# Optimization experiments

Hardware: AMD Instinct MI355X
Metric: run time of the kernel (lower is better)

## Reference

```python
import jax, jax.numpy as jnp
import numpy as np

B, S, D_IN, D, H, HD, HALF, L = 64, 500, 64, 128, 8, 16, 5, 2
WIN = 2 * HALF + 1  # 11 attended positions per query
EPS = 1e-12  # HF layer_norm_eps default


def _ln(x, g, b):
    m = x.mean(-1, keepdims=True)
    v = ((x - m) ** 2).mean(-1, keepdims=True)
    return (x - m) / jnp.sqrt(v + EPS) * g + b


def setup_inputs() -> dict:
    key = jax.random.key(0)
    ks = jax.random.split(key, 24)
    n = lambda i, shape: jax.random.normal(ks[i], shape, jnp.float32) * 0.02
    return {
        "x": jax.random.normal(ks[0], (B, S, D_IN), jnp.float32),
        "W_in": n(1, (D_IN, D)), "b_in": jnp.zeros((D,), jnp.float32),
        "pos_emb": n(2, (512, D)), "tt_emb": n(3, (D,)),
        "ln_emb_g": jnp.ones((D,), jnp.float32), "ln_emb_b": jnp.zeros((D,), jnp.float32),
        "Wq": n(4, (L, D, D)), "bq": jnp.zeros((L, D), jnp.float32),
        "Wk": n(5, (L, D, D)), "bk": jnp.zeros((L, D), jnp.float32),
        "Wv": n(6, (L, D, D)), "bv": jnp.zeros((L, D), jnp.float32),
        "Wo": n(7, (L, D, D)), "bo": jnp.zeros((L, D), jnp.float32),
        "ln1_g": jnp.ones((L, D), jnp.float32), "ln1_b": jnp.zeros((L, D), jnp.float32),
        "Wi": n(8, (L, D, 512)), "bi": jnp.zeros((L, 512), jnp.float32),
        "Wo2": n(9, (L, 512, D)), "bo2": jnp.zeros((L, D), jnp.float32),
        "ln2_g": jnp.ones((L, D), jnp.float32), "ln2_b": jnp.zeros((L, D), jnp.float32),
        "W_cls": n(10, (D, 2)), "b_cls": jnp.zeros((2,), jnp.float32),
    }


def reference(x, W_in, b_in, pos_emb, tt_emb, ln_emb_g, ln_emb_b,
              Wq, bq, Wk, bk, Wv, bv, Wo, bo, ln1_g, ln1_b,
              Wi, bi, Wo2, bo2, ln2_g, ln2_b, W_cls, b_cls):
    # input projection + RoBERTa-style embeddings (position ids start at padding_idx+1=2)
    h = x @ W_in + b_in
    pos_ids = 2 + jnp.arange(S)
    h = _ln(h + pos_emb[pos_ids] + tt_emb, ln_emb_g, ln_emb_b)

    # sliding-window gather indices: each query attends [i-HALF, i+HALF]
    idx = jnp.arange(S)[:, None] + jnp.arange(-HALF, HALF + 1)[None, :]
    valid = (idx >= 0) & (idx < S)
    idxc = jnp.clip(idx, 0, S - 1)
    scale = 1.0 / jnp.sqrt(jnp.float32(HD))

    for l in range(L):
        qh = (h @ Wq[l] + bq[l]).reshape(B, S, H, HD).transpose(0, 2, 1, 3)
        kh = (h @ Wk[l] + bk[l]).reshape(B, S, H, HD).transpose(0, 2, 1, 3)
        vh = (h @ Wv[l] + bv[l]).reshape(B, S, H, HD).transpose(0, 2, 1, 3)
        kk = kh[:, :, idxc]
        scores = jnp.einsum('bhsd,bhswd->bhsw', qh * scale, kk)
        scores = jnp.where(valid, scores, -jnp.inf)
        probs = jax.nn.softmax(scores, axis=-1)
        vv = vh[:, :, idxc]
        ctx = jnp.einsum('bhsw,bhswd->bhsd', probs, vv)
        ctx = ctx.transpose(0, 2, 1, 3).reshape(B, S, D)
        h = _ln(ctx @ Wo[l] + bo[l] + h, ln1_g[l], ln1_b[l])
        ff = jax.nn.gelu(h @ Wi[l] + bi[l], approximate=False) @ Wo2[l] + bo2[l]
        h = _ln(ff + h, ln2_g[l], ln2_b[l])

    pooled = h.mean(axis=1)  # mean over sequence
    return pooled @ W_cls + b_cls
```

## Files before the change

kernel.cpp:

```cpp
#include <hip/hip_runtime.h>
#include <hip/hip_bf16.h>
#include <math.h>

#define BB 64
#define SS 500
#define DIN 64
#define DD 128
#define HH 8
#define HDIM 16
#define HALF_ 5
#define WINW 11
#define LL 2
#define FF 512
#define MM (BB*SS)
#define LN_EPS 1e-12f

typedef __attribute__((ext_vector_type(8))) short short8;
typedef __attribute__((ext_vector_type(4))) float f32x4;

__global__ __launch_bounds__(256) void k_prep(
    const float* __restrict__ Wq, const float* __restrict__ Wk,
    const float* __restrict__ Wv, const float* __restrict__ Wo,
    const float* __restrict__ Wi, const float* __restrict__ Wo2,
    const float* __restrict__ Win, __hip_bfloat16* __restrict__ wT)
{
    const int m = blockIdx.y;
    const float* src; int Kd, Nd, kshift, doff;
    if (m == 12) {
        src = Win; Kd = 64; Nd = 128; kshift = 6; doff = 393216;
    } else {
        const int l = m / 6, t = m % 6;
        int toff;
        switch (t) {
          case 0:  src = Wq  + l*16384; Kd=128; Nd=128; kshift=7; toff=0;      break;
          case 1:  src = Wk  + l*16384; Kd=128; Nd=128; kshift=7; toff=16384;  break;
          case 2:  src = Wv  + l*16384; Kd=128; Nd=128; kshift=7; toff=32768;  break;
          case 3:  src = Wo  + l*16384; Kd=128; Nd=128; kshift=7; toff=49152;  break;
          case 4:  src = Wi  + l*65536; Kd=128; Nd=512; kshift=7; toff=65536;  break;
          default: src = Wo2 + l*65536; Kd=512; Nd=128; kshift=9; toff=131072; break;
        }
        doff = l*196608 + toff;
    }
    __hip_bfloat16* dst = wT + doff;
    const int NK = Kd * Nd;
    int e = (blockIdx.x * 256 + threadIdx.x) * 4;
    if (e >= NK) return;
    #pragma unroll
    for (int j = 0; j < 4; ++j, ++e) {
        int n = e >> kshift, kx = e & (Kd - 1);
        dst[(size_t)n * Kd + kx] = __float2bfloat16(src[(size_t)kx * Nd + n]);
    }
}

__global__ __launch_bounds__(256) void k_xcvt(
    const float* __restrict__ x, __hip_bfloat16* __restrict__ xbf)
{
    int i = (blockIdx.x * 256 + threadIdx.x) * 4;
    if (i >= MM * DIN) return;
    float4 v = *(const float4*)(x + i);
    ushort4 o;
    __hip_bfloat16 t0 = __float2bfloat16(v.x); o.x = *(unsigned short*)&t0;
    __hip_bfloat16 t1 = __float2bfloat16(v.y); o.y = *(unsigned short*)&t1;
    __hip_bfloat16 t2 = __float2bfloat16(v.z); o.z = *(unsigned short*)&t2;
    __hip_bfloat16 t3 = __float2bfloat16(v.w); o.w = *(unsigned short*)&t3;
    *(ushort4*)(xbf + i) = o;
}

#define GEMM_MAIN(Abf, lda, Kdim, WTbf, ldw, n0w)                             \
    __shared__ __align__(16) __hip_bfloat16 As[64][72];                       \
    __shared__ __align__(16) __hip_bfloat16 Ws[128][72];                      \
    const int tid = threadIdx.x;                                              \
    const int wid = tid >> 6;                                                 \
    const int l15 = tid & 15;                                                 \
    const int l4  = (tid & 63) >> 4;                                          \
    const int m0  = blockIdx.x * 64;                                          \
    f32x4 acc[8];                                                             \
    _Pragma("unroll")                                                         \
    for (int n = 0; n < 8; ++n) acc[n] = (f32x4){0.f, 0.f, 0.f, 0.f};         \
    for (int k0 = 0; k0 < (Kdim); k0 += 64) {                                 \
        _Pragma("unroll")                                                     \
        for (int it = 0; it < 2; ++it) {                                      \
            int lin = it * 2048 + tid * 8;                                    \
            int r = lin >> 6, c = lin & 63;                                   \
            *(uint4*)&As[r][c] =                                              \
                *(const uint4*)((Abf) + (size_t)(m0 + r) * (lda) + k0 + c);   \
        }                                                                     \
        _Pragma("unroll")                                                     \
        for (int it = 0; it < 4; ++it) {                                      \
            int lin = it * 2048 + tid * 8;                                    \
            int r = lin >> 6, c = lin & 63;                                   \
            *(uint4*)&Ws[r][c] =                                              \
                *(const uint4*)((WTbf) + (size_t)((n0w) + r) * (ldw) + k0 + c); \
        }                                                                     \
        __syncthreads();                                                      \
        _Pragma("unroll")                                                     \
        for (int kc = 0; kc < 64; kc += 32) {                                 \
            short8 a0 = *(const short8*)&As[wid * 16 + l15][kc + l4 * 8];     \
            _Pragma("unroll")                                                 \
            for (int n = 0; n < 8; ++n) {                                     \
                short8 bf = *(const short8*)&Ws[n * 16 + l15][kc + l4 * 8];   \
                acc[n] = __builtin_amdgcn_mfma_f32_16x16x32_bf16(a0, bf, acc[n], 0, 0, 0); \
            }                                                                 \
        }                                                                     \
        __syncthreads();                                                      \
    }

__global__ __launch_bounds__(256, 4) void k_embed(
    const __hip_bfloat16* __restrict__ xbf, const __hip_bfloat16* __restrict__ wInT,
    const float* __restrict__ bin, const float* __restrict__ pos,
    const float* __restrict__ tt, const float* __restrict__ g,
    const float* __restrict__ be, float* __restrict__ h,
    __hip_bfloat16* __restrict__ hbf)
{
    GEMM_MAIN(xbf, DIN, DIN, wInT, DIN, 0)
    #pragma unroll
    for (int qq = 0; qq < 4; ++qq) {
        const int row = m0 + wid * 16 + l4 * 4 + qq;
        const int s = row % SS;
        float vals[8]; float s1 = 0.f, s2 = 0.f;
        #pragma unroll
        for (int n = 0; n < 8; ++n) {
            const int col = n * 16 + l15;
            float val = acc[n][qq] + bin[col] + tt[col] + pos[(size_t)(2 + s) * DD + col];
            vals[n] = val; s1 += val; s2 += val * val;
        }
        #pragma unroll
        for (int o = 1; o < 16; o <<= 1) {
            s1 += __shfl_xor(s1, o, 16);
            s2 += __shfl_xor(s2, o, 16);
        }
        const float mean = s1 * (1.0f / DD);
        const float var  = s2 * (1.0f / DD) - mean * mean;
        const float rstd = rsqrtf(var + LN_EPS);
        #pragma unroll
        for (int n = 0; n < 8; ++n) {
            const int col = n * 16 + l15;
            const float o = (vals[n] - mean) * rstd * g[col] + be[col];
            h[(size_t)row * DD + col]   = o;
            hbf[(size_t)row * DD + col] = __float2bfloat16(o);
        }
    }
}

__global__ __launch_bounds__(512, 4) void k_fused(
    const __hip_bfloat16* __restrict__ hin,
    const __hip_bfloat16* __restrict__ wTq, const __hip_bfloat16* __restrict__ wTk,
    const __hip_bfloat16* __restrict__ wTv, const __hip_bfloat16* __restrict__ wTo,
    const float* __restrict__ bq, const float* __restrict__ bk,
    const float* __restrict__ bv, const float* __restrict__ bo,
    const float* __restrict__ hres,
    const float* __restrict__ g1, const float* __restrict__ bt1,
    float* __restrict__ hout, __hip_bfloat16* __restrict__ hbfout)
{
    __shared__ __align__(16) char smem[48896];
    __hip_bfloat16* kS   = (__hip_bfloat16*)smem;
    __hip_bfloat16* vS   = (__hip_bfloat16*)(smem + 13056);
    __hip_bfloat16* hS   = (__hip_bfloat16*)(smem + 26112);
    __hip_bfloat16* qS   = (__hip_bfloat16*)(smem + 39168);
    float*          rsum = (float*)(smem + 47872);
    __hip_bfloat16* ctxS = hS;

    const int tid = threadIdx.x;
    const int wid = tid >> 6;
    const int l15 = tid & 15, l4 = (tid & 63) >> 4;
    const int b = blockIdx.y;
    const int s0 = blockIdx.x * 32;

    #pragma unroll
    for (int it = 0; it < 2; ++it) {
        int lin = it * 512 + tid;
        if (lin < 768) {
            int r = lin >> 4, c8 = (lin & 15) * 8;
            int s = s0 - 5 + r;
            uint4 val = {0, 0, 0, 0};
            if (s >= 0 && s < SS)
                val = *(const uint4*)(hin + ((size_t)(b * SS + s)) * DD + c8);
            *(uint4*)&hS[r * 136 + c8] = val;
        }
    }
    __syncthreads();

    #pragma unroll
    for (int i = 0; i < 9; ++i) {
        const int t = wid + i * 8;
        const int out = t / 24;
        const int rem = t - out * 24;
        const int rt = rem >> 3, n = rem & 7;
        const __hip_bfloat16* WT = (out == 0) ? wTq : ((out == 1) ? wTk : wTv);
        const float* bias = (out == 0) ? bq : ((out == 1) ? bk : bv);
        f32x4 a = (f32x4){0.f, 0.f, 0.f, 0.f};
        #pragma unroll
        for (int kc = 0; kc < 4; ++kc) {
            short8 af  = *(const short8*)&hS[(rt * 16 + l15) * 136 + kc * 32 + l4 * 8];
            short8 bfg = *(const short8*)(WT + (size_t)(n * 16 + l15) * DD + kc * 32 + l4 * 8);
            a = __builtin_amdgcn_mfma_f32_16x16x32_bf16(af, bfg, a, 0, 0, 0);
        }
        const int col = n * 16 + l15;
        const float bcol = bias[col];
        #pragma unroll
        for (int qq = 0; qq < 4; ++qq) {
            const int row = rt * 16 + l4 * 4 + qq;
            const float val = a[qq] + bcol;
            if (out == 0) {
                if (row >= 5 && row < 37)
                    qS[(row - 5) * 136 + col] = __float2bfloat16(val * 0.25f);
            } else if (out == 1) {
                kS[row * 136 + col] = __float2bfloat16(val);
            } else {
                vS[row * 136 + col] = __float2bfloat16(val);
            }
        }
    }
    __syncthreads();

    {
        const int g = tid >> 4, wl = tid & 15;
        const int sq = s0 + g;
        const int sk = sq + wl - HALF_;
        const bool valid = (wl < WINW) && (sq < SS) && (sk >= 0) && (sk < SS);
        #pragma unroll
        for (int hh = 0; hh < 8; ++hh) {
            const int off = hh * 16;
            const uint4* qp = (const uint4*)&qS[g * 136 + off];
            const uint4* kp = (const uint4*)&kS[(g + wl) * 136 + off];
            uint4 qv0 = qp[0], qv1 = qp[1];
            uint4 kv0 = kp[0], kv1 = kp[1];
            float sc = 0.f;
            #define DOTD(qu, ku)                                              \
                sc += __uint_as_float((qu) << 16) * __uint_as_float((ku) << 16) \
                    + __uint_as_float((qu) & 0xffff0000u) * __uint_as_float((ku) & 0xffff0000u);
            DOTD(qv0.x, kv0.x) DOTD(qv0.y, kv0.y) DOTD(qv0.z, kv0.z) DOTD(qv0.w, kv0.w)
            DOTD(qv1.x, kv1.x) DOTD(qv1.y, kv1.y) DOTD(qv1.z, kv1.z) DOTD(qv1.w, kv1.w)
            #undef DOTD
            sc = valid ? sc : -INFINITY;
            float mx = sc;
            #pragma unroll
            for (int o = 1; o < 16; o <<= 1) mx = fmaxf(mx, __shfl_xor(mx, o, 16));
            float p = valid ? __expf(sc - mx) : 0.f;
            float den = p;
            #pragma unroll
            for (int o = 1; o < 16; o <<= 1) den += __shfl_xor(den, o, 16);
            const float inv = (den > 0.f) ? 1.f / den : 0.f;
            float cd = 0.f;
            #pragma unroll
            for (int w2 = 0; w2 < WINW; ++w2)
                cd += __shfl(p, w2, 16) * __bfloat162float(vS[(g + w2) * 136 + off + wl]);
            ctxS[g * 136 + off + wl] = __float2bfloat16(cd * inv);
        }
    }
    __syncthreads();

    const int rt2 = wid & 1, nh = wid >> 1;
    f32x4 ac[2];
    #pragma unroll
    for (int n4 = 0; n4 < 2; ++n4) {
        ac[n4] = (f32x4){0.f, 0.f, 0.f, 0.f};
        const int n = nh * 2 + n4;
        #pragma unroll
        for (int kc = 0; kc < 4; ++kc) {
            short8 af  = *(const short8*)&ctxS[(rt2 * 16 + l15) * 136 + kc * 32 + l4 * 8];
            short8 bfg = *(const short8*)(wTo + (size_t)(n * 16 + l15) * DD + kc * 32 + l4 * 8);
            ac[n4] = __builtin_amdgcn_mfma_f32_16x16x32_bf16(af, bfg, ac[n4], 0, 0, 0);
        }
    }
    float vals[4][2];
    #pragma unroll
    for (int qq = 0; qq < 4; ++qq) {
        const int r16 = l4 * 4 + qq;
        const int qrow = rt2 * 16 + r16;
        const int sq = s0 + qrow;
        const bool vr = (sq < SS);
        float s1 = 0.f, s2 = 0.f;
        #pragma unroll
        for (int n4 = 0; n4 < 2; ++n4) {
            const int col = (nh * 2 + n4) * 16 + l15;
            const float resv = vr ? hres[((size_t)(b * SS + sq)) * DD + col] : 0.f;
            const float val = ac[n4][qq] + bo[col] + resv;
            vals[qq][n4] = val; s1 += val; s2 += val * val;
        }
        #pragma unroll
        for (int o = 1; o < 16; o <<= 1) {
            s1 += __shfl_xor(s1, o, 16);
            s2 += __shfl_xor(s2, o, 16);
        }
        if (l15 == 0) {
            rsum[((rt2 * 4 + nh) * 16 + r16) * 2]     = s1;
            rsum[((rt2 * 4 + nh) * 16 + r16) * 2 + 1] = s2;
        }
    }
    __syncthreads();
    #pragma unroll
    for (int qq = 0; qq < 4; ++qq) {
        const int r16 = l4 * 4 + qq;
        const int qrow = rt2 * 16 + r16;
        const int sq = s0 + qrow;
        if (sq >= SS) continue;
        float S1 = 0.f, S2 = 0.f;
        #pragma unroll
        for (int j = 0; j < 4; ++j) {
            S1 += rsum[((rt2 * 4 + j) * 16 + r16) * 2];
            S2 += rsum[((rt2 * 4 + j) * 16 + r16) * 2 + 1];
        }
        const float mean = S1 * (1.0f / DD);
        const float var  = S2 * (1.0f / DD) - mean * mean;
        const float rstd = rsqrtf(fmaxf(var, 0.f) + LN_EPS);
        #pragma unroll
        for (int n4 = 0; n4 < 2; ++n4) {
            const int col = (nh * 2 + n4) * 16 + l15;
            const float o = (vals[qq][n4] - mean) * rstd * g1[col] + bt1[col];
            hout[((size_t)(b * SS + sq)) * DD + col]   = o;
            hbfout[((size_t)(b * SS + sq)) * DD + col] = __float2bfloat16(o);
        }
    }
}

__global__ __launch_bounds__(256, 4) void k_gemm_gelu(
    const __hip_bfloat16* __restrict__ hbf,
    const __hip_bfloat16* __restrict__ wTi,
    const float* __restrict__ bias, __hip_bfloat16* __restrict__ hid)
{
    const int n0g = blockIdx.y * 128;
    GEMM_MAIN(hbf, DD, DD, wTi, DD, n0g)
    #pragma unroll
    for (int qq = 0; qq < 4; ++qq) {
        const int row = m0 + wid * 16 + l4 * 4 + qq;
        #pragma unroll
        for (int n = 0; n < 8; ++n) {
            const int col = n0g + n * 16 + l15;
            float val = acc[n][qq] + bias[col];
            val = 0.5f * val * (1.f + erff(val * 0.70710678118f));
            hid[(size_t)row * FF + col] = __float2bfloat16(val);
        }
    }
}

__global__ __launch_bounds__(256, 4) void k_gemm_lnres(
    const __hip_bfloat16* __restrict__ Abf, int lda, int Kdim,
    const __hip_bfloat16* __restrict__ WT,
    const float* __restrict__ bias, const float* __restrict__ res,
    const float* __restrict__ g, const float* __restrict__ bt,
    float* __restrict__ outF, __hip_bfloat16* __restrict__ outB)
{
    GEMM_MAIN(Abf, lda, Kdim, WT, Kdim, 0)
    #pragma unroll
    for (int qq = 0; qq < 4; ++qq) {
        const int row = m0 + wid * 16 + l4 * 4 + qq;
        float vals[8]; float s1 = 0.f, s2 = 0.f;
        #pragma unroll
        for (int n = 0; n < 8; ++n) {
            const int col = n * 16 + l15;
            float val = acc[n][qq] + bias[col] + res[(size_t)row * DD + col];
            vals[n] = val; s1 += val; s2 += val * val;
        }
        #pragma unroll
        for (int o = 1; o < 16; o <<= 1) {
            s1 += __shfl_xor(s1, o, 16);
            s2 += __shfl_xor(s2, o, 16);
        }
        const float mean = s1 * (1.0f / DD);
        const float var  = s2 * (1.0f / DD) - mean * mean;
        const float rstd = rsqrtf(var + LN_EPS);
        #pragma unroll
        for (int n = 0; n < 8; ++n) {
            const int col = n * 16 + l15;
            const float o = (vals[n] - mean) * rstd * g[col] + bt[col];
            outF[(size_t)row * DD + col] = o;
            outB[(size_t)row * DD + col] = __float2bfloat16(o);
        }
    }
}

__global__ __launch_bounds__(512) void k_final(
    const float* __restrict__ h, const float* __restrict__ Wc,
    const float* __restrict__ bc, float* __restrict__ out)
{
    const int b = blockIdx.x;
    const int tid = threadIdx.x;
    const int d = tid & 127, sg = tid >> 7;
    __shared__ float red[4][128];
    __shared__ float r2[8][2];

    float p = 0.f;
    for (int s = sg; s < SS; s += 4)
        p += h[((size_t)(b * SS + s)) * DD + d];
    red[sg][d] = p;
    __syncthreads();

    float l0 = 0.f, l1 = 0.f;
    if (sg == 0) {
        const float tot = (red[0][d] + red[1][d] + red[2][d] + red[3][d]) * (1.0f / SS);
        l0 = tot * Wc[d * 2 + 0];
        l1 = tot * Wc[d * 2 + 1];
    }
    #pragma unroll
    for (int off = 1; off < 64; off <<= 1) {
        l0 += __shfl_xor(l0, off);
        l1 += __shfl_xor(l1, off);
    }
    const int w = tid >> 6;
    if ((tid & 63) == 0) { r2[w][0] = l0; r2[w][1] = l1; }
    __syncthreads();
    if (tid == 0) {
        out[b * 2 + 0] = r2[0][0] + r2[1][0] + bc[0];
        out[b * 2 + 1] = r2[0][1] + r2[1][1] + bc[1];
    }
}

extern "C" void kernel_launch(void* const* d_in, const int* in_sizes, int n_in,
                              void* d_out, int out_size, void* d_ws, size_t ws_size,
                              hipStream_t stream)
{
    const float* x      = (const float*)d_in[0];
    const float* W_in   = (const float*)d_in[1];
    const float* b_in   = (const float*)d_in[2];
    const float* pos    = (const float*)d_in[3];
    const float* tt     = (const float*)d_in[4];
    const float* lng    = (const float*)d_in[5];
    const float* lnb    = (const float*)d_in[6];
    const float* Wq     = (const float*)d_in[7];
    const float* bq     = (const float*)d_in[8];
    const float* Wk     = (const float*)d_in[9];
    const float* bk     = (const float*)d_in[10];
    const float* Wv     = (const float*)d_in[11];
    const float* bv     = (const float*)d_in[12];
    const float* Wo     = (const float*)d_in[13];
    const float* bo     = (const float*)d_in[14];
    const float* ln1g   = (const float*)d_in[15];
    const float* ln1b   = (const float*)d_in[16];
    const float* Wi     = (const float*)d_in[17];
    const float* bi     = (const float*)d_in[18];
    const float* Wo2    = (const float*)d_in[19];
    const float* bo2    = (const float*)d_in[20];
    const float* ln2g   = (const float*)d_in[21];
    const float* ln2b   = (const float*)d_in[22];
    const float* Wc     = (const float*)d_in[23];
    const float* bc     = (const float*)d_in[24];

    float*          ws   = (float*)d_ws;
    float*          hA   = ws;
    __hip_bfloat16* hbA  = (__hip_bfloat16*)(ws + 4096000);
    __hip_bfloat16* xbf  = (__hip_bfloat16*)(ws + 6144000);
    __hip_bfloat16* wT   = (__hip_bfloat16*)(ws + 7168000);
    __hip_bfloat16* hid  = (__hip_bfloat16*)(ws + 7368704);
    float*          hB   = ws + 15560704;
    __hip_bfloat16* hbB  = (__hip_bfloat16*)(ws + 19656704);

    k_prep<<<dim3(64, 13), 256, 0, stream>>>(Wq, Wk, Wv, Wo, Wi, Wo2, W_in, wT);
    k_xcvt<<<2000, 256, 0, stream>>>(x, xbf);
    k_embed<<<MM / 64, 256, 0, stream>>>(xbf, wT + 393216, b_in, pos, tt, lng, lnb,
                                         hA, hbA);

    float* hI = hA; __hip_bfloat16* hbI = hbA;
    float* hO = hB; __hip_bfloat16* hbO = hbB;
    for (int l = 0; l < LL; ++l) {
        const __hip_bfloat16* wTq  = wT + l * 196608;
        const __hip_bfloat16* wTk  = wTq + 16384;
        const __hip_bfloat16* wTv  = wTq + 32768;
        const __hip_bfloat16* wTo  = wTq + 49152;
        const __hip_bfloat16* wTi  = wTq + 65536;
        const __hip_bfloat16* wTo2 = wTq + 131072;

        k_fused<<<dim3(16, BB), 512, 0, stream>>>(
            hbI, wTq, wTk, wTv, wTo,
            bq + l * DD, bk + l * DD, bv + l * DD, bo + l * DD,
            hI, ln1g + l * DD, ln1b + l * DD, hO, hbO);

        k_gemm_gelu<<<dim3(MM / 64, 4), 256, 0, stream>>>(
            hbO, wTi, bi + l * FF, hid);

        k_gemm_lnres<<<dim3(MM / 64, 1), 256, 0, stream>>>(
            hid, FF, FF, wTo2, bo2 + l * DD, hO, ln2g + l * DD, ln2b + l * DD,
            hO, hbO);

        float* tf = hI; hI = hO; hO = tf;
        __hip_bfloat16* tb = hbI; hbI = hbO; hbO = tb;
    }

    k_final<<<BB, 512, 0, stream>>>(hI, Wc, bc, (float*)d_out);
}
```

Baseline: 362.3 us.

## Fuse FFN up-projection, GELU and down-projection into one kernel via LDS

Replaces the separate GELU GEMM and LN-residual GEMM kernels with one fused FFN kernel. The 512-wide hidden activation is computed in two 256-column halves, kept in shared memory and consumed immediately by the down-projection. This removes the global round trip of the hidden tensor and one launch per layer. It also drops the global-memory A-tile staging of GEMM_MAIN, and weight B fragments are read straight from global memory. A second change in the attention kernel replaces the shuffle-based broadcast of softmax probabilities with a small shared-memory buffer and uses scalar dword loads for the q·k dot product.

Result: no change. 369.1 us (+1.9%).

```diff
diff --git a/kernel.cpp b/kernel.cpp
--- a/kernel.cpp
+++ b/kernel.cpp
@@ -152,12 +152,13 @@
     const float* __restrict__ g1, const float* __restrict__ bt1,
     float* __restrict__ hout, __hip_bfloat16* __restrict__ hbfout)
 {
-    __shared__ __align__(16) char smem[48896];
+    __shared__ __align__(16) char smem[51072];
     __hip_bfloat16* kS   = (__hip_bfloat16*)smem;
     __hip_bfloat16* vS   = (__hip_bfloat16*)(smem + 13056);
     __hip_bfloat16* hS   = (__hip_bfloat16*)(smem + 26112);
     __hip_bfloat16* qS   = (__hip_bfloat16*)(smem + 39168);
-    float*          rsum = (float*)(smem + 47872);
+    float*          pS   = (float*)(smem + 47872);
+    float*          rsum = (float*)(smem + 50048);
     __hip_bfloat16* ctxS = hS;
 
     const int tid = threadIdx.x;
@@ -221,17 +222,15 @@
         #pragma unroll
         for (int hh = 0; hh < 8; ++hh) {
             const int off = hh * 16;
-            const uint4* qp = (const uint4*)&qS[g * 136 + off];
-            const uint4* kp = (const uint4*)&kS[(g + wl) * 136 + off];
-            uint4 qv0 = qp[0], qv1 = qp[1];
-            uint4 kv0 = kp[0], kv1 = kp[1];
             float sc = 0.f;
-            #define DOTD(qu, ku)                                              \
-                sc += __uint_as_float((qu) << 16) * __uint_as_float((ku) << 16) \
-                    + __uint_as_float((qu) & 0xffff0000u) * __uint_as_float((ku) & 0xffff0000u);
-            DOTD(qv0.x, kv0.x) DOTD(qv0.y, kv0.y) DOTD(qv0.z, kv0.z) DOTD(qv0.w, kv0.w)
-            DOTD(qv1.x, kv1.x) DOTD(qv1.y, kv1.y) DOTD(qv1.z, kv1.z) DOTD(qv1.w, kv1.w)
-            #undef DOTD
+            const unsigned* qp = (const unsigned*)&qS[g * 136 + off];
+            const unsigned* kp = (const unsigned*)&kS[(g + wl) * 136 + off];
+            #pragma unroll
+            for (int d2 = 0; d2 < 8; ++d2) {
+                unsigned qu = qp[d2], ku = kp[d2];
+                sc += __uint_as_float(qu << 16) * __uint_as_float(ku << 16)
+                    + __uint_as_float(qu & 0xffff0000u) * __uint_as_float(ku & 0xffff0000u);
+            }
             sc = valid ? sc : -INFINITY;
             float mx = sc;
             #pragma unroll
@@ -241,10 +240,11 @@
             #pragma unroll
             for (int o = 1; o < 16; o <<= 1) den += __shfl_xor(den, o, 16);
             const float inv = (den > 0.f) ? 1.f / den : 0.f;
+            pS[g * 17 + wl] = p;
             float cd = 0.f;
             #pragma unroll
             for (int w2 = 0; w2 < WINW; ++w2)
-                cd += __shfl(p, w2, 16) * __bfloat162float(vS[(g + w2) * 136 + off + wl]);
+                cd += pS[g * 17 + w2] * __bfloat162float(vS[(g + w2) * 136 + off + wl]);
             ctxS[g * 136 + off + wl] = __float2bfloat16(cd * inv);
         }
     }
@@ -314,34 +314,68 @@
     }
 }
 
-__global__ __launch_bounds__(256, 4) void k_gemm_gelu(
-    const __hip_bfloat16* __restrict__ hbf,
-    const __hip_bfloat16* __restrict__ wTi,
-    const float* __restrict__ bias, __hip_bfloat16* __restrict__ hid)
-{
-    const int n0g = blockIdx.y * 128;
-    GEMM_MAIN(hbf, DD, DD, wTi, DD, n0g)
-    #pragma unroll
-    for (int qq = 0; qq < 4; ++qq) {
-        const int row = m0 + wid * 16 + l4 * 4 + qq;
+__global__ __launch_bounds__(256, 4) void k_ffn(
+    const __hip_bfloat16* __restrict__ h1bf,
+    const __hip_bfloat16* __restrict__ wTi, const __hip_bfloat16* __restrict__ wTo2,
+    const float* __restrict__ bi, const float* __restrict__ bo2,
+    const float* __restrict__ res,
+    const float* __restrict__ g2, const float* __restrict__ bt2,
+    float* __restrict__ outF, __hip_bfloat16* __restrict__ outB)
+{
+    __shared__ __align__(16) __hip_bfloat16 h1S[64][136];
+    __shared__ __align__(16) __hip_bfloat16 hidS[64][264];
+    const int tid = threadIdx.x;
+    const int wid = tid >> 6;
+    const int l15 = tid & 15, l4 = (tid & 63) >> 4;
+    const int m0 = blockIdx.x * 64;
+
+    #pragma unroll
+    for (int it = 0; it < 4; ++it) {
+        int lin = it * 256 + tid;
+        int r = lin >> 4, c8 = (lin & 15) * 8;
+        *(uint4*)&h1S[r][c8] = *(const uint4*)(h1bf + (size_t)(m0 + r) * DD + c8);
+    }
+    __syncthreads();
+
+    f32x4 a2[8];
+    #pragma unroll
+    for (int n = 0; n < 8; ++n) a2[n] = (f32x4){0.f, 0.f, 0.f, 0.f};
+
+    for (int half = 0; half < 2; ++half) {
+        #pragma unroll
+        for (int i = 0; i < 16; ++i) {
+            const int t = wid + i * 4;
+            const int rt = t >> 4, nloc = t & 15;
+            const int n = half * 16 + nloc;
+            f32x4 a = (f32x4){0.f, 0.f, 0.f, 0.f};
+            #pragma unroll
+            for (int kc = 0; kc < 4; ++kc) {
+                short8 af  = *(const short8*)&h1S[rt * 16 + l15][kc * 32 + l4 * 8];
+                short8 bfg = *(const short8*)(wTi + (size_t)(n * 16 + l15) * DD + kc * 32 + l4 * 8);
+                a = __builtin_amdgcn_mfma_f32_16x16x32_bf16(af, bfg, a, 0, 0, 0);
+            }
+            const float bcol = bi[n * 16 + l15];
+            #pragma unroll
+            for (int qq = 0; qq < 4; ++qq) {
+                float val = a[qq] + bcol;
+                val = 0.5f * val * (1.f + erff(val * 0.70710678118f));
+                hidS[rt * 16 + l4 * 4 + qq][nloc * 16 + l15] = __float2bfloat16(val);
+            }
+        }
+        __syncthreads();
         #pragma unroll
         for (int n = 0; n < 8; ++n) {
-            const int col = n0g + n * 16 + l15;
-            float val = acc[n][qq] + bias[col];
-            val = 0.5f * val * (1.f + erff(val * 0.70710678118f));
-            hid[(size_t)row * FF + col] = __float2bfloat16(val);
-        }
-    }
-}
-
-__global__ __launch_bounds__(256, 4) void k_gemm_lnres(
-    const __hip_bfloat16* __restrict__ Abf, int lda, int Kdim,
-    const __hip_bfloat16* __restrict__ WT,
-    const float* __restrict__ bias, const float* __restrict__ res,
-    const float* __restrict__ g, const float* __restrict__ bt,
-    float* __restrict__ outF, __hip_bfloat16* __restrict__ outB)
-{
-    GEMM_MAIN(Abf, lda, Kdim, WT, Kdim, 0)
+            #pragma unroll
+            for (int ksl = 0; ksl < 8; ++ksl) {
+                short8 af  = *(const short8*)&hidS[wid * 16 + l15][ksl * 32 + l4 * 8];
+                short8 bfg = *(const short8*)(wTo2 + (size_t)(n * 16 + l15) * FF
+                                              + half * 256 + ksl * 32 + l4 * 8);
+                a2[n] = __builtin_amdgcn_mfma_f32_16x16x32_bf16(af, bfg, a2[n], 0, 0, 0);
+            }
+        }
+        __syncthreads();
+    }
+
     #pragma unroll
     for (int qq = 0; qq < 4; ++qq) {
         const int row = m0 + wid * 16 + l4 * 4 + qq;
@@ -349,7 +383,7 @@
         #pragma unroll
         for (int n = 0; n < 8; ++n) {
             const int col = n * 16 + l15;
-            float val = acc[n][qq] + bias[col] + res[(size_t)row * DD + col];
+            float val = a2[n][qq] + bo2[col] + res[(size_t)row * DD + col];
             vals[n] = val; s1 += val; s2 += val * val;
         }
         #pragma unroll
@@ -363,7 +397,7 @@
         #pragma unroll
         for (int n = 0; n < 8; ++n) {
             const int col = n * 16 + l15;
-            const float o = (vals[n] - mean) * rstd * g[col] + bt[col];
+            const float o = (vals[n] - mean) * rstd * g2[col] + bt2[col];
             outF[(size_t)row * DD + col] = o;
             outB[(size_t)row * DD + col] = __float2bfloat16(o);
         }
@@ -441,9 +475,8 @@
     __hip_bfloat16* hbA  = (__hip_bfloat16*)(ws + 4096000);
     __hip_bfloat16* xbf  = (__hip_bfloat16*)(ws + 6144000);
     __hip_bfloat16* wT   = (__hip_bfloat16*)(ws + 7168000);
-    __hip_bfloat16* hid  = (__hip_bfloat16*)(ws + 7368704);
-    float*          hB   = ws + 15560704;
-    __hip_bfloat16* hbB  = (__hip_bfloat16*)(ws + 19656704);
+    float*          hB   = ws + 7368704;
+    __hip_bfloat16* hbB  = (__hip_bfloat16*)(ws + 11464704);
 
     k_prep<<<dim3(64, 13), 256, 0, stream>>>(Wq, Wk, Wv, Wo, Wi, Wo2, W_in, wT);
     k_xcvt<<<2000, 256, 0, stream>>>(x, xbf);
@@ -465,12 +498,9 @@
             bq + l * DD, bk + l * DD, bv + l * DD, bo + l * DD,
             hI, ln1g + l * DD, ln1b + l * DD, hO, hbO);
 
-        k_gemm_gelu<<<dim3(MM / 64, 4), 256, 0, stream>>>(
-            hbO, wTi, bi + l * FF, hid);
-
-        k_gemm_lnres<<<dim3(MM / 64, 1), 256, 0, stream>>>(
-            hid, FF, FF, wTo2, bo2 + l * DD, hO, ln2g + l * DD, ln2b + l * DD,
-            hO, hbO);
+        k_ffn<<<MM / 64, 256, 0, stream>>>(
+            hbO, wTi, wTo2, bi + l * FF, bo2 + l * DD,
+            hO, ln2g + l * DD, ln2b + l * DD, hO, hbO);
 
         float* tf = hI; hI = hO; hO = tf;
         __hip_bfloat16* tb = hbI; hbI = hbO; hbO = tb;
```
